# Performance work log

Hardware: AMD Instinct MI355X
Metric: run time of the kernel (lower is better)

Reference implementation:

```python
import jax, jax.numpy as jnp
import numpy as np

K_TOP = 2          # hardcoded k in MyAttentionFunction
S = 32             # hardcoded spatial size (interpolate to 32x32)
N = S * S          # 1024 patches (patch_size=1, stride=1 unfold)
NEG = jnp.float32(-1e30)  # stand-in for excluding columns from top-k


def setup_inputs() -> dict:
    key = jax.random.key(0)
    k1, k2, k3 = jax.random.split(key, 3)
    C = 4096
    generated = jax.random.normal(k1, (1, C, S, S), dtype=jnp.float32)
    known = jax.random.normal(k2, (1, C, S, S), dtype=jnp.float32)
    mask = jax.random.randint(k3, (1, 1, S, S), 0, 2).astype(jnp.float32)
    return {"generated": generated, "known": known, "mask": mask}


def _forward(generated, known, mask):
    C = generated.shape[1]
    # F.interpolate(mask, (32,32)) nearest, then flatten -> flag in {0,1}, shape (N,)
    flag = jax.image.resize(mask, (1, 1, S, S), method="nearest").reshape(N)
    # MyUnfold(x, 1, 1) == [1, N, C]; drop batch dim of 1.
    P = generated.reshape(C, N).T   # (N, C) patches of `generated`
    Kp = known.reshape(C, N).T      # (N, C) patches of `known`

    norm_p = jnp.sum(P * P, axis=-1)   # (N,)
    norm_k = jnp.sum(Kp * Kp, axis=-1)
    # Full cosine matrices; original restricts rows to flag==1 and columns to
    # flag==0 (cosine0) / flag==1 (cosine1) by extraction; we mask columns with
    # a very negative value so top-k returns the same values with GLOBAL indices
    # (which is exactly what the original reconstructs via nonzero()[indexes]).
    cos0 = (P @ Kp.T) / jnp.sqrt(norm_p[:, None] * norm_k[None, :])  # (N, N)
    cos1 = (P @ P.T) / jnp.sqrt(norm_p[:, None] * norm_p[None, :])
    cos0 = jnp.where(flag[None, :] == 0, cos0, NEG)
    cos1 = jnp.where(flag[None, :] == 1, cos1, NEG)

    w0, i0 = jax.lax.top_k(cos0, K_TOP)  # (N, k) values / global indices
    w1, i1 = jax.lax.top_k(cos1, K_TOP)

    m = flag                      # 1.0 on masked rows
    nm = jnp.sum(m)               # number of masked patches
    # weight means taken only over masked rows, then softmax (original uses
    # .item() + numpy softmax, i.e. detached constants).
    means = jnp.stack(
        [jnp.sum(w0[:, i] * m) / nm for i in range(K_TOP)]
        + [jnp.sum(w1[:, i] * m) / nm for i in range(K_TOP)]
    )
    weights = jax.lax.stop_gradient(jax.nn.softmax(means))  # (2k,)

    # The original builds dense 1024x1024 indicator matrices and bmm's them;
    # each indicator row for a masked patch is one-hot at its retrieved source,
    # so the bmm is just a gather into masked rows. The advanced-indexing quirk
    # ind[mask_idx, src_idx] (nonzero() pairs include a leading 0 column) also
    # unconditionally sets ind[0,0]=1; we reproduce that (set semantics: no
    # double count if row 0 already maps to column 0).
    rtn = jnp.zeros((N, C), dtype=generated.dtype)
    for i in range(2 * K_TOP):
        src = Kp if i < K_TOP else P
        cols = (i0 if i < K_TOP else i1)[:, i % K_TOP]  # (N,) global indices
        out_i = jnp.where(m[:, None] == 1, src[cols], 0.0)  # masked rows only
        dup = 1.0 - ((m[0] == 1) & (cols[0] == 0)).astype(src.dtype)
        out_i = out_i.at[0].add(src[0] * dup)  # spurious ind[0,0]=1 artifact
        rtn = rtn + weights[i] * out_i

    rtn = rtn.reshape(1, S, S, C).transpose(0, 3, 1, 2)  # (1, C, 32, 32)
    return jnp.concatenate([generated, known, rtn], axis=1)


def reference(generated, known, mask):
    return _forward(generated, known, mask)
```

## Files before the change

kernel.cpp:

```cpp
#include <hip/hip_runtime.h>
#include <hip/hip_bf16.h>
#include <math.h>

#define N_TOT 1024
#define C_DIM 4096
#define T_MARGIN 3e-4f

typedef __attribute__((ext_vector_type(8))) _Float16 half8;
typedef __attribute__((ext_vector_type(8))) unsigned short ushort8;
typedef __attribute__((ext_vector_type(8))) char schar8;
typedef __attribute__((ext_vector_type(4))) float floatx4;

__device__ inline unsigned short f2h(float v) {
    _Float16 h = (_Float16)v;
    return __builtin_bit_cast(unsigned short, h);
}
__device__ inline float h2f(unsigned short u) {
    return (float)__builtin_bit_cast(_Float16, u);
}
__device__ inline char lo_enc(float v, unsigned short h) {
    int e = (h >> 10) & 31;
    float lo = v - h2f(h);
    float q = rintf(lo * 240.0f * __uint_as_float((unsigned)(152 - e) << 23));
    q = fmaxf(-127.0f, fminf(127.0f, q));
    return (char)(int)q;
}
__device__ inline float lo_dec(char q, unsigned short h) {
    int e = (h >> 10) & 31;
    return (float)q * __uint_as_float((unsigned)(e + 102) << 23) * (1.0f / 240.0f);
}

__device__ inline void ins2(float v, int s, float& v1, int& s1, float& v2, int& s2) {
    if (v > v1 || (v == v1 && s < s1)) { v2 = v1; s2 = s1; v1 = v; s1 = s; }
    else if (v > v2 || (v == v2 && s < s2)) { v2 = v; s2 = s; }
}

__global__ __launch_bounds__(256) void split_norms(const float* __restrict__ G,
                                                   const float* __restrict__ Kn,
                                                   const float* __restrict__ flag,
                                                   unsigned short* __restrict__ Phi,
                                                   char* __restrict__ Plo,
                                                   unsigned short* __restrict__ Khi,
                                                   char* __restrict__ Klo,
                                                   float* __restrict__ normP,
                                                   float* __restrict__ normK,
                                                   int* __restrict__ colidx,
                                                   int* __restrict__ n0p) {
    const int z = blockIdx.z;
    const float* X = z ? Kn : G;
    unsigned short* Xhi = z ? Khi : Phi;
    char* Xlo = z ? Klo : Plo;
    float* normX = z ? normK : normP;

    __shared__ float tile[64 * 65];
    const int t  = threadIdx.x;
    const int c0 = blockIdx.x * 64;
    const int n0 = blockIdx.y * 64;

    #pragma unroll
    for (int s = 0; s < 4; s++) {
        int c_loc = s * 16 + (t >> 4);
        int n4    = (t & 15) * 4;
        float4 v = *(const float4*)&X[(size_t)(c0 + c_loc) * N_TOT + n0 + n4];
        tile[c_loc * 65 + n4 + 0] = v.x;
        tile[c_loc * 65 + n4 + 1] = v.y;
        tile[c_loc * 65 + n4 + 2] = v.z;
        tile[c_loc * 65 + n4 + 3] = v.w;
    }
    __syncthreads();

    #pragma unroll
    for (int s = 0; s < 2; s++) {
        int n_loc = s * 32 + (t >> 3);
        int c8    = (t & 7) * 8;
        unsigned short h[8]; char l[8];
        float s2 = 0.0f;
        #pragma unroll
        for (int e = 0; e < 8; e++) {
            float v = tile[(c8 + e) * 65 + n_loc];
            s2 = fmaf(v, v, s2);
            h[e] = f2h(v);
            l[e] = lo_enc(v, h[e]);
        }
        s2 += __shfl_xor(s2, 1);
        s2 += __shfl_xor(s2, 2);
        s2 += __shfl_xor(s2, 4);
        if ((t & 7) == 0) atomicAdd(&normX[n0 + n_loc], s2);

        size_t base = (size_t)(n0 + n_loc) * C_DIM + c0 + c8;
        ushort8 hv; schar8 lv;
        #pragma unroll
        for (int e = 0; e < 8; e++) { hv[e] = h[e]; lv[e] = l[e]; }
        *(ushort8*)&Xhi[base] = hv;
        *(schar8*)&Xlo[base]  = lv;
    }

    if (blockIdx.x == 0 && blockIdx.y == 0 && blockIdx.z == 0) {
        __shared__ int cz[256];
        __shared__ int co[256];
        float4 fv = *(const float4*)&flag[4 * t];
        int f[4] = {fv.x == 0.0f, fv.y == 0.0f, fv.z == 0.0f, fv.w == 0.0f};
        int nz = f[0] + f[1] + f[2] + f[3];
        cz[t] = nz; co[t] = 4 - nz;
        __syncthreads();
        for (int off = 1; off < 256; off <<= 1) {
            int vz = (t >= off) ? cz[t - off] : 0;
            int vo = (t >= off) ? co[t - off] : 0;
            __syncthreads();
            cz[t] += vz; co[t] += vo;
            __syncthreads();
        }
        const int fn0 = cz[255];
        int zs = cz[t] - nz;
        int os = fn0 + co[t] - (4 - nz);
        #pragma unroll
        for (int e = 0; e < 4; e++) {
            int j = 4 * t + e;
            if (f[e]) colidx[zs++] = j;
            else      colidx[os++] = j;
        }
        if (t == 0) *n0p = fn0;
    }
}

__global__ __launch_bounds__(256, 2) void gemm_coarse(const unsigned short* __restrict__ Phi,
                                                      const unsigned short* __restrict__ Khi,
                                                      const int* __restrict__ colidx,
                                                      const int* __restrict__ n0p,
                                                      float* __restrict__ dotPart) {
    __shared__ unsigned short sA[128 * 64];
    __shared__ unsigned short sB[128 * 64];

    const int t    = threadIdx.x;
    const int wave = t >> 6, lane = t & 63;
    const int wm   = wave >> 1, wn = wave & 1;
    const int quad = lane >> 4, lrow = lane & 15;
    const int ib = blockIdx.x * 128, jb = blockIdx.y * 128;
    const int bz = blockIdx.z;
    const int k_beg = bz * 512;
    const int n0 = *n0p;

    const int srow = t >> 3;
    const int g    = (t & 7) ^ (srow & 7);

    const unsigned short* gA0 = Phi + (size_t)(ib + srow) * C_DIM + g * 8;
    const unsigned short* gB[4];
    #pragma unroll
    for (int q = 0; q < 4; q++) {
        int s = jb + q * 32 + srow;
        int row = colidx[s];
        const unsigned short* src = (s < n0) ? Khi : Phi;
        gB[q] = src + (size_t)row * C_DIM + g * 8;
    }

    floatx4 acc[4][4] = {};

    for (int k0 = k_beg; k0 < k_beg + 512; k0 += 64) {
        #pragma unroll
        for (int q = 0; q < 4; q++)
            __builtin_amdgcn_global_load_lds(
                (const __attribute__((address_space(1))) void*)(gA0 + (size_t)q * 32 * C_DIM + k0),
                (__attribute__((address_space(3))) void*)((char*)sA + q * 4096 + t * 16), 16, 0, 0);
        #pragma unroll
        for (int q = 0; q < 4; q++)
            __builtin_amdgcn_global_load_lds(
                (const __attribute__((address_space(1))) void*)(gB[q] + k0),
                (__attribute__((address_space(3))) void*)((char*)sB + q * 4096 + t * 16), 16, 0, 0);
        __syncthreads();

        #pragma unroll
        for (int kk = 0; kk < 2; kk++) {
            const int gk = kk * 4 + quad;
            half8 a[4], b[4];
            #pragma unroll
            for (int ti = 0; ti < 4; ti++) {
                int m = wm * 64 + ti * 16 + lrow;
                a[ti] = *(const half8*)&sA[m * 64 + ((gk ^ (m & 7)) << 3)];
            }
            #pragma unroll
            for (int tj = 0; tj < 4; tj++) {
                int n = wn * 64 + tj * 16 + lrow;
                b[tj] = *(const half8*)&sB[n * 64 + ((gk ^ (n & 7)) << 3)];
            }
            #pragma unroll
            for (int ti = 0; ti < 4; ti++)
                #pragma unroll
                for (int tj = 0; tj < 4; tj++)
                    acc[ti][tj] = __builtin_amdgcn_mfma_f32_16x16x32_f16(a[ti], b[tj], acc[ti][tj], 0, 0, 0);
        }
        __syncthreads();
    }

    float* outp = dotPart + ((size_t)bz << 20);
    #pragma unroll
    for (int tj = 0; tj < 4; tj++) {
        int j = jb + wn * 64 + tj * 16 + lrow;
        #pragma unroll
        for (int ti = 0; ti < 4; ti++) {
            #pragma unroll
            for (int reg = 0; reg < 4; reg++) {
                int i = ib + wm * 64 + ti * 16 + quad * 4 + reg;
                outp[i * N_TOT + j] = acc[ti][tj][reg];
            }
        }
    }
}

__global__ __launch_bounds__(256) void select_k(const float* __restrict__ dotPart,
                                                const float* __restrict__ normP,
                                                const float* __restrict__ normK,
                                                const int* __restrict__ colidx,
                                                const int* __restrict__ n0p,
                                                float* __restrict__ w01,
                                                int* __restrict__ i01,
                                                int* __restrict__ wl_hdr,
                                                int* __restrict__ wl_cand) {
    __shared__ float sr_v1[2][4], sr_v2[2][4];
    __shared__ int   sr_s1[2][4], sr_s2[2][4];
    __shared__ int   s_cnt[2];
    __shared__ int   s_cand[2][16];

    const int row = blockIdx.x;
    const int t   = threadIdx.x;
    const int wave = t >> 6, lane = t & 63;
    const int n0 = *n0p;
    const float nr = normP[row];

    if (t < 2) s_cnt[t] = 0;

    const float* base = dotPart + (size_t)row * N_TOT + 4 * t;
    float4 p0 = *(const float4*)(base);
    float4 p1 = *(const float4*)(base + (1ull << 20));
    float4 p2 = *(const float4*)(base + (2ull << 20));
    float4 p3 = *(const float4*)(base + (3ull << 20));
    float4 p4 = *(const float4*)(base + (4ull << 20));
    float4 p5 = *(const float4*)(base + (5ull << 20));
    float4 p6 = *(const float4*)(base + (6ull << 20));
    float4 p7 = *(const float4*)(base + (7ull << 20));
    float4 dv;
    dv.x = ((p0.x + p1.x) + (p2.x + p3.x)) + ((p4.x + p5.x) + (p6.x + p7.x));
    dv.y = ((p0.y + p1.y) + (p2.y + p3.y)) + ((p4.y + p5.y) + (p6.y + p7.y));
    dv.z = ((p0.z + p1.z) + (p2.z + p3.z)) + ((p4.z + p5.z) + (p6.z + p7.z));
    dv.w = ((p0.w + p1.w) + (p2.w + p3.w)) + ((p4.w + p5.w) + (p6.w + p7.w));

    float cv[4];
    #pragma unroll
    for (int e = 0; e < 4; e++) {
        int s = 4 * t + e;
        int gj = colidx[s];
        float nb = (s < n0) ? normK[gj] : normP[gj];
        float d  = (e == 0) ? dv.x : (e == 1) ? dv.y : (e == 2) ? dv.z : dv.w;
        cv[e] = d * rsqrtf(nr * nb);
    }

    #pragma unroll
    for (int zz = 0; zz < 2; zz++) {
        float v1 = -INFINITY, v2 = -INFINITY;
        int   s1 = 0x7FFFFFFF, s2 = 0x7FFFFFFF;
        #pragma unroll
        for (int e = 0; e < 4; e++) {
            int s = 4 * t + e;
            bool inz = zz ? (s >= n0) : (s < n0);
            if (inz) ins2(cv[e], s, v1, s1, v2, s2);
        }
        #pragma unroll
        for (int off = 32; off > 0; off >>= 1) {
            float o1 = __shfl_xor(v1, off); int q1 = __shfl_xor(s1, off);
            float o2 = __shfl_xor(v2, off); int q2 = __shfl_xor(s2, off);
            ins2(o1, q1, v1, s1, v2, s2);
            ins2(o2, q2, v1, s1, v2, s2);
        }
        if (lane == 0) {
            sr_v1[zz][wave] = v1; sr_s1[zz][wave] = s1;
            sr_v2[zz][wave] = v2; sr_s2[zz][wave] = s2;
        }
    }
    __syncthreads();

    float m1z[2], m2z[2]; int b1z[2], b2z[2];
    #pragma unroll
    for (int zz = 0; zz < 2; zz++) {
        float m1 = -INFINITY, m2 = -INFINITY;
        int   b1 = 0x7FFFFFFF, b2 = 0x7FFFFFFF;
        #pragma unroll
        for (int w = 0; w < 4; w++) {
            ins2(sr_v1[zz][w], sr_s1[zz][w], m1, b1, m2, b2);
            ins2(sr_v2[zz][w], sr_s2[zz][w], m1, b1, m2, b2);
        }
        m1z[zz] = m1; m2z[zz] = m2; b1z[zz] = b1; b2z[zz] = b2;
        const float thr = m2 - T_MARGIN;
        #pragma unroll
        for (int e = 0; e < 4; e++) {
            int s = 4 * t + e;
            bool inz = zz ? (s >= n0) : (s < n0);
            if (inz && cv[e] > thr) {
                int idx = atomicAdd(&s_cnt[zz], 1);
                if (idx < 16) s_cand[zz][idx] = s;
            }
        }
    }
    __syncthreads();

    bool need[2]; int cntz[2];
    #pragma unroll
    for (int zz = 0; zz < 2; zz++) {
        const int cnt = min(s_cnt[zz], 16);
        cntz[zz] = cnt;
        const bool trusted = (s_cnt[zz] == 2) && (m1z[zz] - m2z[zz] > T_MARGIN);
        need[zz] = !trusted;
        if (t == 0) {
            wl_hdr[2 * row + zz] = trusted ? 0 : cnt;
            if (trusted) {
                int base2 = (zz * N_TOT + row) * 2;
                w01[base2]     = m1z[zz];
                w01[base2 + 1] = m2z[zz];
                i01[base2]     = colidx[b1z[zz]];
                i01[base2 + 1] = colidx[b2z[zz]];
            }
        }
    }
    __syncthreads();

    #pragma unroll
    for (int zz = 0; zz < 2; zz++)
        if (need[zz] && t < cntz[zz])
            wl_cand[(2 * row + zz) * 16 + t] = s_cand[zz][t];
}

__global__ __launch_bounds__(256) void refine2(const unsigned short* __restrict__ Phi,
                                               const char* __restrict__ Plo,
                                               const unsigned short* __restrict__ Khi,
                                               const char* __restrict__ Klo,
                                               const float* __restrict__ normP,
                                               const float* __restrict__ normK,
                                               const int* __restrict__ colidx,
                                               const int* __restrict__ n0p,
                                               const int* __restrict__ wl_hdr,
                                               const int* __restrict__ wl_cand,
                                               float* __restrict__ w01,
                                               int* __restrict__ i01) {
    __shared__ float sAf[C_DIM];
    __shared__ float s_rcv[16];
    __shared__ int   s_rcj[16];

    const int item = blockIdx.x;
    const int cnt  = wl_hdr[item];
    if (cnt == 0) return;

    const int row = item >> 1;
    const int zz  = item & 1;
    const int t   = threadIdx.x;
    const int grp = t >> 5, l32 = t & 31;
    const int n0 = *n0p;
    const float nr = normP[row];

    {
        const unsigned short* Ah = Phi + (size_t)row * C_DIM;
        const char*           Al = Plo + (size_t)row * C_DIM;
        #pragma unroll
        for (int s = 0; s < 2; s++) {
            int c = t * 16 + s * 8;
            ushort8 hb = *(const ushort8*)&Ah[c];
            schar8  lb = *(const schar8*)&Al[c];
            #pragma unroll
            for (int e = 0; e < 8; e++) sAf[c + e] = h2f(hb[e]) + lo_dec(lb[e], hb[e]);
        }
    }
    __syncthreads();

    #pragma unroll
    for (int p = 0; p < 2; p++) {
        if (p == 1 && cnt <= 8) break;
        const int q = grp + 8 * p;
        float acc = 0.0f;
        int gj = 0; float nb = 1.0f;
        if (q < cnt) {
            const int cs = wl_cand[item * 16 + q];
            gj = colidx[cs];
            nb = (cs < n0) ? normK[gj] : normP[gj];
            const unsigned short* bh_row = ((cs < n0) ? Khi : Phi) + (size_t)gj * C_DIM;
            const char*           bl_row = ((cs < n0) ? Klo : Plo) + (size_t)gj * C_DIM;
            #pragma unroll 4
            for (int it = 0; it < 16; it++) {
                int c = it * 256 + l32 * 8;
                ushort8 hb = *(const ushort8*)&bh_row[c];
                schar8  lb = *(const schar8*)&bl_row[c];
                #pragma unroll
                for (int e = 0; e < 8; e++)
                    acc = fmaf(sAf[c + e], h2f(hb[e]) + lo_dec(lb[e], hb[e]), acc);
            }
        }
        #pragma unroll
        for (int off = 16; off > 0; off >>= 1) acc += __shfl_xor(acc, off);
        if (l32 == 0 && q < cnt) {
            s_rcv[q] = acc * rsqrtf(nr * nb);
            s_rcj[q] = gj;
        }
    }
    __syncthreads();

    if (t == 0) {
        float v1 = -INFINITY, v2 = -INFINITY;
        int   j1 = 0x7FFFFFFF, j2 = 0x7FFFFFFF;
        for (int q = 0; q < cnt; q++) {
            float cvx = s_rcv[q];
            int   j   = s_rcj[q];
            if (cvx > v1 || (cvx == v1 && j < j1)) {
                v2 = v1; j2 = j1; v1 = cvx; j1 = j;
            } else if (cvx > v2 || (cvx == v2 && j < j2)) {
                v2 = cvx; j2 = j;
            }
        }
        if (j1 == 0x7FFFFFFF) j1 = 0;
        if (j2 == 0x7FFFFFFF) j2 = j1;
        int base = (zz * N_TOT + row) * 2;
        w01[base]     = v1;
        w01[base + 1] = v2;
        i01[base]     = j1;
        i01[base + 1] = j2;
    }
}

__global__ __launch_bounds__(256) void means_k(const float* __restrict__ flag,
                                               const float* __restrict__ w01,
                                               float* __restrict__ wts) {
    __shared__ float red[5][4];
    const int t = threadIdx.x;
    const int wave = t >> 6, lane = t & 63;

    float pm[5] = {};
    #pragma unroll
    for (int e = 0; e < 4; e++) {
        int n = 4 * t + e;
        float m = flag[n];
        pm[0] += m;
        pm[1] += m * w01[n * 2 + 0];
        pm[2] += m * w01[n * 2 + 1];
        pm[3] += m * w01[2 * N_TOT + n * 2 + 0];
        pm[4] += m * w01[2 * N_TOT + n * 2 + 1];
    }
    #pragma unroll
    for (int i = 0; i < 5; i++)
        #pragma unroll
        for (int off = 32; off > 0; off >>= 1)
            pm[i] += __shfl_xor(pm[i], off);
    if (lane == 0) {
        #pragma unroll
        for (int i = 0; i < 5; i++) red[i][wave] = pm[i];
    }
    __syncthreads();
    if (t == 0) {
        float tot[5];
        #pragma unroll
        for (int i = 0; i < 5; i++)
            tot[i] = red[i][0] + red[i][1] + red[i][2] + red[i][3];
        float inv = 1.0f / tot[0];
        float mv[4] = {tot[1] * inv, tot[2] * inv, tot[3] * inv, tot[4] * inv};
        float mx = fmaxf(fmaxf(mv[0], mv[1]), fmaxf(mv[2], mv[3]));
        float e[4], s = 0.0f;
        #pragma unroll
        for (int q = 0; q < 4; q++) { e[q] = expf(mv[q] - mx); s += e[q]; }
        #pragma unroll
        for (int q = 0; q < 4; q++) wts[q] = e[q] / s;
    }
}

__global__ __launch_bounds__(256) void output_kernel(const float* __restrict__ G,
                                                     const float* __restrict__ Kn,
                                                     const float* __restrict__ flag,
                                                     const int* __restrict__ i01,
                                                     const float* __restrict__ wts,
                                                     float* __restrict__ out) {
    __shared__ float sG[2][N_TOT];
    __shared__ float sKn[2][N_TOT];
    __shared__ float swts[4];
    const int c0 = blockIdx.x * 2;
    const int t  = threadIdx.x;
    const int n4 = t * 4;

    if (t < 4) swts[t] = wts[t];

    #pragma unroll
    for (int ch = 0; ch < 2; ch++) {
        int c = c0 + ch;
        float4 gv = *(const float4*)&G[c * N_TOT + n4];
        float4 kv = *(const float4*)&Kn[c * N_TOT + n4];
        *(float4*)&sG[ch][n4]  = gv;
        *(float4*)&sKn[ch][n4] = kv;
        *(float4*)&out[c * N_TOT + n4] = gv;
        *(float4*)&out[C_DIM * N_TOT + c * N_TOT + n4] = kv;
    }

    float4 fv = *(const float4*)&flag[n4];
    const float fa[4] = {fv.x, fv.y, fv.z, fv.w};
    __syncthreads();

    const float w0 = swts[0], w1 = swts[1], w2 = swts[2], w3 = swts[3];

    float val[2][4];
    #pragma unroll
    for (int e = 0; e < 4; e++) {
        int n = n4 + e;
        float v0 = 0.0f, v1 = 0.0f;
        if (fa[e] == 1.0f) {
            int2 i0 = *(const int2*)&i01[n * 2];
            int2 i1 = *(const int2*)&i01[2 * N_TOT + n * 2];
            v0 = w0 * sKn[0][i0.x] + w1 * sKn[0][i0.y]
               + w2 * sG[0][i1.x]  + w3 * sG[0][i1.y];
            v1 = w0 * sKn[1][i0.x] + w1 * sKn[1][i0.y]
               + w2 * sG[1][i1.x]  + w3 * sG[1][i1.y];
        }
        if (n == 0) {
            bool m0 = (flag[0] == 1.0f);
            int2 i0 = *(const int2*)&i01[0];
            int2 i1 = *(const int2*)&i01[2 * N_TOT];
            if (!(m0 && i0.x == 0)) { v0 += w0 * sKn[0][0]; v1 += w0 * sKn[1][0]; }
            if (!(m0 && i0.y == 0)) { v0 += w1 * sKn[0][0]; v1 += w1 * sKn[1][0]; }
            if (!(m0 && i1.x == 0)) { v0 += w2 * sG[0][0];  v1 += w2 * sG[1][0]; }
            if (!(m0 && i1.y == 0)) { v0 += w3 * sG[0][0];  v1 += w3 * sG[1][0]; }
        }
        val[0][e] = v0; val[1][e] = v1;
    }
    #pragma unroll
    for (int ch = 0; ch < 2; ch++)
        *(float4*)&out[2 * C_DIM * N_TOT + (c0 + ch) * N_TOT + n4] =
            make_float4(val[ch][0], val[ch][1], val[ch][2], val[ch][3]);
}

extern "C" void kernel_launch(void* const* d_in, const int* in_sizes, int n_in,
                              void* d_out, int out_size, void* d_ws, size_t ws_size,
                              hipStream_t stream) {
    const float* G    = (const float*)d_in[0];
    const float* Kn   = (const float*)d_in[1];
    const float* flag = (const float*)d_in[2];
    float* out = (float*)d_out;

    char* p = (char*)d_ws;
    unsigned short* Phi = (unsigned short*)p;  p += (size_t)N_TOT * C_DIM * 2;
    unsigned short* Khi = (unsigned short*)p;  p += (size_t)N_TOT * C_DIM * 2;
    char* Plo = p;                             p += (size_t)N_TOT * C_DIM;
    char* Klo = p;                             p += (size_t)N_TOT * C_DIM;
    float* dotPart = (float*)p;                p += (size_t)8 * N_TOT * N_TOT * 4;
    float* normP   = (float*)p;                p += N_TOT * 4;
    float* normK   = (float*)p;                p += N_TOT * 4;
    float* wts     = (float*)p;                p += 16;
    float* w01     = (float*)p;                p += 4 * N_TOT * 4;
    int*   i01     = (int*)p;                  p += 4 * N_TOT * 4;
    int*   colidx  = (int*)p;                  p += N_TOT * 4;
    int*   n0p     = (int*)p;                  p += 16;
    int*   wl_hdr  = (int*)p;                  p += 2 * N_TOT * 4;
    int*   wl_cand = (int*)p;

    hipMemsetAsync(normP, 0, 2 * N_TOT * sizeof(float), stream);

    split_norms<<<dim3(64, 16, 2), 256, 0, stream>>>(G, Kn, flag, Phi, Plo, Khi, Klo,
                                                     normP, normK, colidx, n0p);
    gemm_coarse<<<dim3(8, 8, 8), 256, 0, stream>>>(Phi, Khi, colidx, n0p, dotPart);
    select_k<<<1024, 256, 0, stream>>>(dotPart, normP, normK, colidx, n0p,
                                       w01, i01, wl_hdr, wl_cand);
    refine2<<<2048, 256, 0, stream>>>(Phi, Plo, Khi, Klo, normP, normK, colidx, n0p,
                                      wl_hdr, wl_cand, w01, i01);
    means_k<<<1, 256, 0, stream>>>(flag, w01, wts);
    output_kernel<<<2048, 256, 0, stream>>>(G, Kn, flag, i01, wts, out);
}
```

Baseline: 167.3 us.

## Restrict similarity GEMM and selection to masked rows only

The coarse GEMM now gathers only masked rows (flag==1, via colidx beyond n0) into the A tile and early-exits blocks past the masked-row count. select_k and refine2 index compacted rows through colidx, and means/output paths avoid reading w01/i01 for unmasked rows that are no longer written. This roughly halves GEMM and selection work for a random mask, at the cost of an indirect row gather for A.

After: 158.4 us. 5.4% less time.

```diff
diff --git a/kernel.cpp b/kernel.cpp
--- a/kernel.cpp
+++ b/kernel.cpp
@@ -128,6 +128,11 @@
                                                       const int* __restrict__ colidx,
                                                       const int* __restrict__ n0p,
                                                       float* __restrict__ dotPart) {
+    const int n0 = *n0p;
+    const int n1 = N_TOT - n0;
+    const int ib = blockIdx.x * 128;
+    if (ib >= n1) return;
+
     __shared__ unsigned short sA[128 * 64];
     __shared__ unsigned short sB[128 * 64];
 
@@ -135,15 +140,21 @@
     const int wave = t >> 6, lane = t & 63;
     const int wm   = wave >> 1, wn = wave & 1;
     const int quad = lane >> 4, lrow = lane & 15;
-    const int ib = blockIdx.x * 128, jb = blockIdx.y * 128;
+    const int jb = blockIdx.y * 128;
     const int bz = blockIdx.z;
     const int k_beg = bz * 512;
-    const int n0 = *n0p;
 
     const int srow = t >> 3;
     const int g    = (t & 7) ^ (srow & 7);
 
-    const unsigned short* gA0 = Phi + (size_t)(ib + srow) * C_DIM + g * 8;
+    const unsigned short* gA[4];
+    #pragma unroll
+    for (int q = 0; q < 4; q++) {
+        int r = ib + q * 32 + srow;
+        int rr = (r < n1) ? r : (n1 - 1);
+        int rowA = colidx[n0 + rr];
+        gA[q] = Phi + (size_t)rowA * C_DIM + g * 8;
+    }
     const unsigned short* gB[4];
     #pragma unroll
     for (int q = 0; q < 4; q++) {
@@ -159,7 +170,7 @@
         #pragma unroll
         for (int q = 0; q < 4; q++)
             __builtin_amdgcn_global_load_lds(
-                (const __attribute__((address_space(1))) void*)(gA0 + (size_t)q * 32 * C_DIM + k0),
+                (const __attribute__((address_space(1))) void*)(gA[q] + k0),
                 (__attribute__((address_space(3))) void*)((char*)sA + q * 4096 + t * 16), 16, 0, 0);
         #pragma unroll
         for (int q = 0; q < 4; q++)
@@ -220,15 +231,21 @@
     __shared__ int   s_cnt[2];
     __shared__ int   s_cand[2][16];
 
-    const int row = blockIdx.x;
-    const int t   = threadIdx.x;
+    const int r = blockIdx.x;
+    const int t = threadIdx.x;
+    const int n0 = *n0p;
+    const int n1 = N_TOT - n0;
+    if (r >= n1) {
+        if (t < 2) wl_hdr[2 * r + t] = 0;
+        return;
+    }
+    const int row = colidx[n0 + r];
     const int wave = t >> 6, lane = t & 63;
-    const int n0 = *n0p;
     const float nr = normP[row];
 
     if (t < 2) s_cnt[t] = 0;
 
-    const float* base = dotPart + (size_t)row * N_TOT + 4 * t;
+    const float* base = dotPart + (size_t)r * N_TOT + 4 * t;
     float4 p0 = *(const float4*)(base);
     float4 p1 = *(const float4*)(base + (1ull << 20));
     float4 p2 = *(const float4*)(base + (2ull << 20));
@@ -309,7 +326,7 @@
         const bool trusted = (s_cnt[zz] == 2) && (m1z[zz] - m2z[zz] > T_MARGIN);
         need[zz] = !trusted;
         if (t == 0) {
-            wl_hdr[2 * row + zz] = trusted ? 0 : cnt;
+            wl_hdr[2 * r + zz] = trusted ? 0 : cnt;
             if (trusted) {
                 int base2 = (zz * N_TOT + row) * 2;
                 w01[base2]     = m1z[zz];
@@ -324,7 +341,7 @@
     #pragma unroll
     for (int zz = 0; zz < 2; zz++)
         if (need[zz] && t < cntz[zz])
-            wl_cand[(2 * row + zz) * 16 + t] = s_cand[zz][t];
+            wl_cand[(2 * r + zz) * 16 + t] = s_cand[zz][t];
 }
 
 __global__ __launch_bounds__(256) void refine2(const unsigned short* __restrict__ Phi,
@@ -347,11 +364,12 @@
     const int cnt  = wl_hdr[item];
     if (cnt == 0) return;
 
-    const int row = item >> 1;
-    const int zz  = item & 1;
+    const int n0 = *n0p;
+    const int r  = item >> 1;
+    const int zz = item & 1;
+    const int row = colidx[n0 + r];
     const int t   = threadIdx.x;
     const int grp = t >> 5, l32 = t & 31;
-    const int n0 = *n0p;
     const float nr = normP[row];
 
     {
@@ -432,12 +450,13 @@
     #pragma unroll
     for (int e = 0; e < 4; e++) {
         int n = 4 * t + e;
-        float m = flag[n];
-        pm[0] += m;
-        pm[1] += m * w01[n * 2 + 0];
-        pm[2] += m * w01[n * 2 + 1];
-        pm[3] += m * w01[2 * N_TOT + n * 2 + 0];
-        pm[4] += m * w01[2 * N_TOT + n * 2 + 1];
+        if (flag[n] == 1.0f) {
+            pm[0] += 1.0f;
+            pm[1] += w01[n * 2 + 0];
+            pm[2] += w01[n * 2 + 1];
+            pm[3] += w01[2 * N_TOT + n * 2 + 0];
+            pm[4] += w01[2 * N_TOT + n * 2 + 1];
+        }
     }
     #pragma unroll
     for (int i = 0; i < 5; i++)
@@ -512,8 +531,8 @@
         }
         if (n == 0) {
             bool m0 = (flag[0] == 1.0f);
-            int2 i0 = *(const int2*)&i01[0];
-            int2 i1 = *(const int2*)&i01[2 * N_TOT];
+            int2 i0 = m0 ? *(const int2*)&i01[0]        : make_int2(-1, -1);
+            int2 i1 = m0 ? *(const int2*)&i01[2 * N_TOT] : make_int2(-1, -1);
             if (!(m0 && i0.x == 0)) { v0 += w0 * sKn[0][0]; v1 += w0 * sKn[1][0]; }
             if (!(m0 && i0.y == 0)) { v0 += w1 * sKn[0][0]; v1 += w1 * sKn[1][0]; }
             if (!(m0 && i1.x == 0)) { v0 += w2 * sG[0][0];  v1 += w2 * sG[1][0]; }
```
